# Performance work log

Hardware: AMD Instinct MI355X
Metric: run time of the kernel (lower is better)

## Reference

```python
import jax, jax.numpy as jnp
import numpy as np

H = W = D = 128   # output volume resolution
GS = 3            # control grid size per axis
N = GS * GS * GS  # 27 control points
B = 2


def _build_constants():
    # Sampling grid: matches np.meshgrid(linspace(w), linspace(h), linspace(d)) in __init__
    gX, gY, gZ = np.meshgrid(np.linspace(-1, 1, W), np.linspace(-1, 1, H), np.linspace(-1, 1, D))
    grid = np.stack([gX, gY, gZ], axis=-1).astype(np.float32)  # (H,W,D,3)
    # Control points: P_Y, P_X, P_Z = np.meshgrid(ax, ax, ax), reshaped (-1,1)
    ax = np.linspace(-1, 1, GS)
    P_Y, P_X, P_Z = np.meshgrid(ax, ax, ax)
    P = np.stack([P_X.reshape(-1), P_Y.reshape(-1), P_Z.reshape(-1)], axis=1).astype(np.float32)  # (N,3)
    # TPS L matrix and its inverse (compute_L_inverse)
    d2 = ((P[:, None, :] - P[None, :, :]) ** 2).sum(-1)
    d2[d2 == 0] = 1.0
    K = d2 * np.log(d2)
    Pm = np.concatenate([np.ones((N, 1), np.float32), P], axis=1)  # (N,4)
    L = np.zeros((N + 4, N + 4), np.float64)
    L[:N, :N] = K
    L[:N, N:] = Pm
    L[N:, :N] = Pm.T
    Li = np.linalg.inv(L).astype(np.float32)  # (N+4, N+4)
    return grid, P, Li


def setup_inputs() -> dict:
    key = jax.random.key(0)
    grid, P, Li = _build_constants()
    theta = jax.random.normal(key, (B, 3 * N), dtype=jnp.float32)
    return {"theta": theta, "grid": jnp.asarray(grid), "P": jnp.asarray(P), "Li": jnp.asarray(Li)}


def reference(theta, grid, P, Li):
    b = theta.shape[0]
    n = P.shape[0]
    # theta[:, :N]=Q_X, theta[:, N:2N]=Q_Y, theta[:, 2N:]=Q_Z -> (B,3,N)
    Q = theta.reshape(b, 3, n)
    Wc = jnp.einsum('nm,bcm->bcn', Li[:n, :n], Q)   # (B,3,N) RBF weights
    Ac = jnp.einsum('am,bcm->bca', Li[n:, :n], Q)   # (B,3,4) affine part
    # Squared distances from every grid point to every control point: (H,W,D,N)
    dx = grid[..., 0, None] - P[:, 0]
    dy = grid[..., 1, None] - P[:, 1]
    dz = grid[..., 2, None] - P[:, 2]
    r2 = dx * dx + dy * dy + dz * dz
    r2 = jnp.where(r2 == 0, 1.0, r2)
    U = r2 * jnp.log(r2)  # TPS kernel r^2 log r^2, (H,W,D,N)
    nonlin = jnp.einsum('hwdn,bcn->bhwdc', U, Wc)               # (B,H,W,D,3)
    affine = Ac[:, None, None, None, :, 0] + jnp.einsum('hwda,bca->bhwdc', grid, Ac[:, :, 1:])
    return affine + nonlin  # (B,H,W,D,3) warped grid
```

## Files before the change

### kernel.cpp

```cpp
#include <hip/hip_runtime.h>
#include <math.h>


#define NP 27
#define NV 31

__global__ __launch_bounds__(192) void tps_prep(
    const float* __restrict__ theta,
    const float* __restrict__ Li,
    float* __restrict__ V)
{
    int t = threadIdx.x;
    if (t >= 6 * NV) return;
    int bc = t / NV;
    int k  = t % NV;
    const float* q  = theta + bc * NP;
    const float* lr = Li + k * NV;
    float acc = 0.f;
    #pragma unroll
    for (int m = 0; m < NP; ++m) acc = fmaf(lr[m], q[m], acc);
    if (k < NP) acc *= 0.69314718055994531f;
    V[t] = acc;
}

__global__ __launch_bounds__(256) void tps_main(
    const float* __restrict__ V,
    float* __restrict__ out)
{
    const int idx = blockIdx.x * 256 + threadIdx.x;
    const int d = idx & 127;
    const int w = (idx >> 7) & 127;
    const int h = idx >> 14;

    const float s = 1.0f / 127.0f;
    const float gx = (float)(2 * w - 127) * s;
    const float gy = (float)(2 * h - 127) * s;
    const float gz = (float)(2 * d - 127) * s;

    float ex[3], ey[3], ez[3];
    ex[0] = (gx + 1.f) * (gx + 1.f); ex[1] = gx * gx; ex[2] = (gx - 1.f) * (gx - 1.f);
    ey[0] = (gy + 1.f) * (gy + 1.f); ey[1] = gy * gy; ey[2] = (gy - 1.f) * (gy - 1.f);
    ez[0] = (gz + 1.f) * (gz + 1.f); ez[1] = gz * gz; ez[2] = (gz - 1.f) * (gz - 1.f);

    float U[NP + 1];
    #pragma unroll
    for (int i = 0; i < 3; ++i) {
        #pragma unroll
        for (int j = 0; j < 3; ++j) {
            const float exy = ex[i] + ey[j];
            #pragma unroll
            for (int k = 0; k < 3; ++k) {
                float r2 = exy + ez[k];
                r2 = fmaxf(r2, 1e-37f);
                U[i * 9 + j * 3 + k] = r2 * __log2f(r2);
            }
        }
    }
    U[NP] = 1.0f;

    const int HWD = 1 << 21;
    #pragma unroll
    for (int b = 0; b < 2; ++b) {
        float o[3];
        #pragma unroll
        for (int c = 0; c < 3; ++c) {
            const float* v = V + (b * 3 + c) * NV;
            float acc = gx * v[NP + 1];
            acc = fmaf(gy, v[NP + 2], acc);
            acc = fmaf(gz, v[NP + 3], acc);
            #pragma unroll
            for (int n = 0; n < NP + 1; ++n) acc = fmaf(U[n], v[n], acc);
            o[c] = acc;
        }
        float* op = out + ((size_t)(b * HWD + idx)) * 3;
        op[0] = o[0]; op[1] = o[1]; op[2] = o[2];
    }
}

extern "C" void kernel_launch(void* const* d_in, const int* in_sizes, int n_in,
                              void* d_out, int out_size, void* d_ws, size_t ws_size,
                              hipStream_t stream) {
    const float* theta = (const float*)d_in[0];
    const float* Li    = (const float*)d_in[3];
    float* V   = (float*)d_ws;
    float* out = (float*)d_out;

    tps_prep<<<1, 192, 0, stream>>>(theta, Li, V);
    tps_main<<<(1 << 21) / 256, 256, 0, stream>>>(V, out);
}
```

Baseline: 100.1 us.

## Process four points per thread with packed FMAs and vectorized stores

Each thread now handles four consecutive depth points. The x/y distance terms are shared across those points, and the weight accumulation uses inline-asm v_pk_fma_f32 with duplicated scalar weights that the prep kernel writes into the workspace. Output is written as three 16-byte vector stores per batch instead of scalar stores, and the grid shrinks by a factor of four. This targets the FMA/VALU work and the store instruction count, at the cost of more registers per thread and fewer threads in flight.

```diff
diff --git a/kernel.cpp b/kernel.cpp
--- a/kernel.cpp
+++ b/kernel.cpp
@@ -3,77 +3,134 @@
 
 
 #define NP 27
-#define NV 31
+
+typedef float v2f __attribute__((ext_vector_type(2)));
+typedef float v4f __attribute__((ext_vector_type(4)));
+
+#define PKFMA(acc, u2, vv) \
+    asm("v_pk_fma_f32 %0, %1, %2, %0" : "+v"(acc) : "v"(u2), "s"(vv))
 
 __global__ __launch_bounds__(192) void tps_prep(
     const float* __restrict__ theta,
     const float* __restrict__ Li,
-    float* __restrict__ V)
+    float* __restrict__ Vd)
 {
     int t = threadIdx.x;
-    if (t >= 6 * NV) return;
-    int bc = t / NV;
-    int k  = t % NV;
-    const float* q  = theta + bc * NP;
-    const float* lr = Li + k * NV;
+    if (t >= 6 * 32) return;
+    int bc = t >> 5;
+    int k  = t & 31;
     float acc = 0.f;
-    #pragma unroll
-    for (int m = 0; m < NP; ++m) acc = fmaf(lr[m], q[m], acc);
-    if (k < NP) acc *= 0.69314718055994531f;
-    V[t] = acc;
+    if (k < 31) {
+        const float* q  = theta + bc * NP;
+        const float* lr = Li + k * 31;
+        #pragma unroll
+        for (int m = 0; m < NP; ++m) acc = fmaf(lr[m], q[m], acc);
+        if (k < NP) acc *= 0.69314718055994531f;
+    }
+    Vd[2 * t]     = acc;
+    Vd[2 * t + 1] = acc;
 }
 
 __global__ __launch_bounds__(256) void tps_main(
-    const float* __restrict__ V,
+    const float* __restrict__ Vd,
     float* __restrict__ out)
 {
-    const int idx = blockIdx.x * 256 + threadIdx.x;
-    const int d = idx & 127;
-    const int w = (idx >> 7) & 127;
-    const int h = idx >> 14;
+    const int t = blockIdx.x * 256 + threadIdx.x;
+    const int base = t << 2;
+    const int d0 = base & 127;
+    const int w = (base >> 7) & 127;
+    const int h = base >> 14;
 
     const float s = 1.0f / 127.0f;
     const float gx = (float)(2 * w - 127) * s;
     const float gy = (float)(2 * h - 127) * s;
-    const float gz = (float)(2 * d - 127) * s;
+    float gz[4];
+    #pragma unroll
+    for (int p = 0; p < 4; ++p) gz[p] = (float)(2 * (d0 + p) - 127) * s;
 
-    float ex[3], ey[3], ez[3];
+    float ex[3], ey[3];
     ex[0] = (gx + 1.f) * (gx + 1.f); ex[1] = gx * gx; ex[2] = (gx - 1.f) * (gx - 1.f);
     ey[0] = (gy + 1.f) * (gy + 1.f); ey[1] = gy * gy; ey[2] = (gy - 1.f) * (gy - 1.f);
-    ez[0] = (gz + 1.f) * (gz + 1.f); ez[1] = gz * gz; ez[2] = (gz - 1.f) * (gz - 1.f);
 
-    float U[NP + 1];
+    v2f exy[9];
     #pragma unroll
-    for (int i = 0; i < 3; ++i) {
+    for (int i = 0; i < 3; ++i)
         #pragma unroll
         for (int j = 0; j < 3; ++j) {
-            const float exy = ex[i] + ey[j];
+            float e = (ex[i] + ey[j]) + 1e-37f;
+            exy[i * 3 + j] = (v2f){e, e};
+        }
+
+    v2f ez[2][3];
+    #pragma unroll
+    for (int q = 0; q < 2; ++q) {
+        float a = gz[2 * q], b = gz[2 * q + 1];
+        ez[q][0] = (v2f){(a + 1.f) * (a + 1.f), (b + 1.f) * (b + 1.f)};
+        ez[q][1] = (v2f){a * a, b * b};
+        ez[q][2] = (v2f){(a - 1.f) * (a - 1.f), (b - 1.f) * (b - 1.f)};
+    }
+
+    const v2f* __restrict__ VV = (const v2f*)Vd;
+
+    v2f acc[2][2][3];
+    #pragma unroll
+    for (int b = 0; b < 2; ++b)
+        #pragma unroll
+        for (int c = 0; c < 3; ++c) {
+            const float* vr = (const float*)(VV + (b * 3 + c) * 32);
+            float a28 = vr[2 * 28], a29 = vr[2 * 29], a30 = vr[2 * 30];
+            float ab = fmaf(gy, a29, gx * a28);
+            #pragma unroll
+            for (int q = 0; q < 2; ++q)
+                acc[q][b][c] = (v2f){fmaf(gz[2 * q],     a30, ab),
+                                     fmaf(gz[2 * q + 1], a30, ab)};
+        }
+
+    #pragma unroll
+    for (int i = 0; i < 3; ++i)
+        #pragma unroll
+        for (int j = 0; j < 3; ++j)
             #pragma unroll
             for (int k = 0; k < 3; ++k) {
-                float r2 = exy + ez[k];
-                r2 = fmaxf(r2, 1e-37f);
-                U[i * 9 + j * 3 + k] = r2 * __log2f(r2);
+                const int n = i * 9 + j * 3 + k;
+                v2f u[2];
+                #pragma unroll
+                for (int q = 0; q < 2; ++q) {
+                    v2f r2 = exy[i * 3 + j] + ez[q][k];
+                    v2f lg;
+                    lg.x = __log2f(r2.x);
+                    lg.y = __log2f(r2.y);
+                    u[q] = r2 * lg;
+                }
+                #pragma unroll
+                for (int b = 0; b < 2; ++b)
+                    #pragma unroll
+                    for (int c = 0; c < 3; ++c)
+                        #pragma unroll
+                        for (int q = 0; q < 2; ++q)
+                            PKFMA(acc[q][b][c], u[q], VV[(b * 3 + c) * 32 + n]);
             }
+
+    #pragma unroll
+    for (int b = 0; b < 2; ++b)
+        #pragma unroll
+        for (int c = 0; c < 3; ++c) {
+            float a27 = ((const float*)(VV + (b * 3 + c) * 32))[2 * 27];
+            v2f a2 = (v2f){a27, a27};
+            #pragma unroll
+            for (int q = 0; q < 2; ++q) acc[q][b][c] = acc[q][b][c] + a2;
         }
-    }
-    U[NP] = 1.0f;
 
     const int HWD = 1 << 21;
     #pragma unroll
     for (int b = 0; b < 2; ++b) {
-        float o[3];
-        #pragma unroll
-        for (int c = 0; c < 3; ++c) {
-            const float* v = V + (b * 3 + c) * NV;
-            float acc = gx * v[NP + 1];
-            acc = fmaf(gy, v[NP + 2], acc);
-            acc = fmaf(gz, v[NP + 3], acc);
-            #pragma unroll
-            for (int n = 0; n < NP + 1; ++n) acc = fmaf(U[n], v[n], acc);
-            o[c] = acc;
-        }
-        float* op = out + ((size_t)(b * HWD + idx)) * 3;
-        op[0] = o[0]; op[1] = o[1]; op[2] = o[2];
+        float* op = out + ((size_t)(b * HWD + base)) * 3;
+        v4f s0 = (v4f){acc[0][b][0].x, acc[0][b][1].x, acc[0][b][2].x, acc[0][b][0].y};
+        v4f s1 = (v4f){acc[0][b][1].y, acc[0][b][2].y, acc[1][b][0].x, acc[1][b][1].x};
+        v4f s2 = (v4f){acc[1][b][2].x, acc[1][b][0].y, acc[1][b][1].y, acc[1][b][2].y};
+        *reinterpret_cast<v4f*>(op)     = s0;
+        *reinterpret_cast<v4f*>(op + 4) = s1;
+        *reinterpret_cast<v4f*>(op + 8) = s2;
     }
 }
 
@@ -86,5 +143,5 @@
     float* out = (float*)d_out;
 
     tps_prep<<<1, 192, 0, stream>>>(theta, Li, V);
-    tps_main<<<(1 << 21) / 256, 256, 0, stream>>>(V, out);
+    tps_main<<<(1 << 21) / 4 / 256, 256, 0, stream>>>(V, out);
 }
```

Result: no change. 101.3 us (+1.2%).
